# Kernel optimization log

Hardware: AMD Instinct MI355X
Metric: run time of the kernel (lower is better)

Reference implementation:

```python
import jax, jax.numpy as jnp
import numpy as np

VOCAB = 50257
DIM = 1024
R = 16
ALPHA = 32
SCALING = ALPHA / R


def setup_inputs() -> dict:
    key = jax.random.key(0)
    k1, k2, k3, k4 = jax.random.split(key, 4)
    input_ids = jax.random.randint(k1, (4, 4096), 0, VOCAB)
    emb_weight = jax.random.normal(k2, (VOCAB, DIM), dtype=jnp.float32)
    lora_A = jax.random.normal(k3, (R, VOCAB), dtype=jnp.float32) * (1.0 / R)
    # original init zeros lora_B; use random values so the LoRA path is exercised
    lora_B = jax.random.normal(k4, (DIM, R), dtype=jnp.float32) * 0.02
    return {"input": input_ids, "emb_weight": emb_weight, "lora_A": lora_A, "lora_B": lora_B}


def reference(input, emb_weight, lora_A, lora_B):
    # orig_out = embedding gather: [B, S, D]
    orig_out = jnp.take(emb_weight, input, axis=0)
    # one_hot @ lora_A.T == gather of lora_A columns: [B, S, r]
    a_rows = jnp.take(lora_A, input, axis=1)          # [r, B, S]
    a_rows = jnp.moveaxis(a_rows, 0, -1)              # [B, S, r]
    lora_out = jnp.einsum('bsr,dr->bsd', a_rows, lora_B) * SCALING
    return orig_out + lora_out
```

## Files before the change

### kernel.cpp

```cpp
#include <hip/hip_runtime.h>
#include <hip/hip_bf16.h>

#define VOCAB 50257
#define DIM   1024
#define R     16
#define SCALING 2.0f
#define TPB   16

typedef float floatx4 __attribute__((ext_vector_type(4)));

__global__ __launch_bounds__(256, 4) void adapted_embedding_kernel(
    const int*   __restrict__ ids,
    const float* __restrict__ emb,
    const float* __restrict__ A,
    const float* __restrict__ B,
    float*       __restrict__ out,
    int n_tokens)
{
    __shared__ float sA[TPB][R];
    __shared__ int   sT[TPB];

    const int tid      = threadIdx.x;
    const int base_tok = blockIdx.x * TPB;

    if (tid < TPB) {
        int g = base_tok + tid;
        sT[tid] = (g < n_tokens) ? ids[g] : 0;
    }
    __syncthreads();

    {
        int ti = tid >> 4;
        int r  = tid & 15;
        sA[ti][r] = A[(size_t)r * VOCAB + sT[ti]];
    }

    const int d0 = tid * 4;
    const float4* B4 = reinterpret_cast<const float4*>(B);
    float4 b[16];
    #pragma unroll
    for (int k = 0; k < 4; ++k)
        #pragma unroll
        for (int q = 0; q < 4; ++q)
            b[k * 4 + q] = B4[(size_t)(d0 + k) * 4 + q];

    __syncthreads();

    #pragma unroll
    for (int ti = 0; ti < TPB; ++ti) {
        int gtok = base_tok + ti;
        if (gtok >= n_tokens) break;
        int tok = sT[ti];

        float a[R];
        #pragma unroll
        for (int r = 0; r < R; ++r) a[r] = sA[ti][r];

        const float4* e4 = reinterpret_cast<const float4*>(emb + (size_t)tok * DIM);
        float4 e = e4[tid];

        float acc[4];
        #pragma unroll
        for (int k = 0; k < 4; ++k) {
            float s = 0.0f;
            #pragma unroll
            for (int q = 0; q < 4; ++q) {
                float4 bb = b[k * 4 + q];
                s += bb.x * a[q * 4 + 0];
                s += bb.y * a[q * 4 + 1];
                s += bb.z * a[q * 4 + 2];
                s += bb.w * a[q * 4 + 3];
            }
            acc[k] = s;
        }

        floatx4 res;
        res.x = e.x + SCALING * acc[0];
        res.y = e.y + SCALING * acc[1];
        res.z = e.z + SCALING * acc[2];
        res.w = e.w + SCALING * acc[3];

        floatx4* o4 = reinterpret_cast<floatx4*>(out + (size_t)gtok * DIM);
        __builtin_nontemporal_store(res, &o4[tid]);
    }
}

extern "C" void kernel_launch(void* const* d_in, const int* in_sizes, int n_in,
                              void* d_out, int out_size, void* d_ws, size_t ws_size,
                              hipStream_t stream) {
    const int*   ids = (const int*)  d_in[0];
    const float* emb = (const float*)d_in[1];
    const float* A   = (const float*)d_in[2];
    const float* B   = (const float*)d_in[3];
    float*       out = (float*)d_out;

    const int n_tokens = in_sizes[0];
    const int grid = (n_tokens + TPB - 1) / TPB;

    adapted_embedding_kernel<<<grid, 256, 0, stream>>>(ids, emb, A, B, out, n_tokens);
}
```

Measured before the change: 287.4 us.

## Double tokens per block and prefetch next embedding row in the token loop

Each block now handles 32 tokens instead of 16, which halves how often each block loads B into registers. The shared token-id array and its barrier are removed, and ids are read directly from global memory. The loop loads the embedding row for token i+1 while computing token i, so the gather latency overlaps with the LoRA arithmetic. The trade-off is more redundant global id loads, extra register pressure from the prefetched float4, and half as many blocks in the grid.

```diff
diff --git a/kernel.cpp b/kernel.cpp
--- a/kernel.cpp
+++ b/kernel.cpp
@@ -5,7 +5,7 @@
 #define DIM   1024
 #define R     16
 #define SCALING 2.0f
-#define TPB   16
+#define TPB   32
 
 typedef float floatx4 __attribute__((ext_vector_type(4)));
 
@@ -18,21 +18,19 @@
     int n_tokens)
 {
     __shared__ float sA[TPB][R];
-    __shared__ int   sT[TPB];
 
     const int tid      = threadIdx.x;
     const int base_tok = blockIdx.x * TPB;
 
-    if (tid < TPB) {
-        int g = base_tok + tid;
-        sT[tid] = (g < n_tokens) ? ids[g] : 0;
-    }
-    __syncthreads();
-
     {
         int ti = tid >> 4;
         int r  = tid & 15;
-        sA[ti][r] = A[(size_t)r * VOCAB + sT[ti]];
+        int g0 = base_tok + ti;
+        int g1 = base_tok + ti + 16;
+        int t0 = (g0 < n_tokens) ? ids[g0] : 0;
+        int t1 = (g1 < n_tokens) ? ids[g1] : 0;
+        sA[ti][r]      = A[(size_t)r * VOCAB + t0];
+        sA[ti + 16][r] = A[(size_t)r * VOCAB + t1];
     }
 
     const int d0 = tid * 4;
@@ -46,18 +44,26 @@
 
     __syncthreads();
 
+    float4 e;
+    {
+        int tok0 = (base_tok < n_tokens) ? ids[base_tok] : 0;
+        e = reinterpret_cast<const float4*>(emb + (size_t)tok0 * DIM)[tid];
+    }
+
     #pragma unroll
     for (int ti = 0; ti < TPB; ++ti) {
         int gtok = base_tok + ti;
         if (gtok >= n_tokens) break;
-        int tok = sT[ti];
+
+        float4 cur = e;
+        if (ti + 1 < TPB && gtok + 1 < n_tokens) {
+            int ntok = ids[gtok + 1];
+            e = reinterpret_cast<const float4*>(emb + (size_t)ntok * DIM)[tid];
+        }
 
         float a[R];
         #pragma unroll
         for (int r = 0; r < R; ++r) a[r] = sA[ti][r];
-
-        const float4* e4 = reinterpret_cast<const float4*>(emb + (size_t)tok * DIM);
-        float4 e = e4[tid];
 
         float acc[4];
         #pragma unroll
@@ -75,10 +81,10 @@
         }
 
         floatx4 res;
-        res.x = e.x + SCALING * acc[0];
-        res.y = e.y + SCALING * acc[1];
-        res.z = e.z + SCALING * acc[2];
-        res.w = e.w + SCALING * acc[3];
+        res.x = cur.x + SCALING * acc[0];
+        res.y = cur.y + SCALING * acc[1];
+        res.z = cur.z + SCALING * acc[2];
+        res.w = cur.w + SCALING * acc[3];
 
         floatx4* o4 = reinterpret_cast<floatx4*>(out + (size_t)gtok * DIM);
         __builtin_nontemporal_store(res, &o4[tid]);
```

Result: no change. 284.1 us (-1.1%).
